# Optimization experiments

Hardware: AMD Instinct MI355X
Metric: run time of the kernel (lower is better)

Reference implementation:

```python
import jax, jax.numpy as jnp
import numpy as np

N, P, T, K = 20000, 5, 16, 3
IN, H, O = 150, 64, 128


def setup_inputs() -> dict:
    key = jax.random.key(0)
    k1, k2, k3, k4, k5 = jax.random.split(key, 5)
    x = jax.random.normal(k1, (N, IN), dtype=jnp.float32)
    conn_idx = jax.random.randint(k2, (N, P, T, K), 0, N, dtype=jnp.int32)
    conn_w = jax.random.uniform(k3, (N, P, T, K), dtype=jnp.float32)
    # learned params
    W1 = jax.random.normal(k4, (H, IN), dtype=jnp.float32) * 0.05   # linear_1 (no bias)
    Wg = jax.random.normal(k5, (O, H, P, T), dtype=jnp.float32) * 0.05  # geodesic conv weight
    bg = jnp.zeros((O,), dtype=jnp.float32)                          # geodesic conv bias
    return {"x": x, "conn_idx": conn_idx, "conn_w": conn_w, "W1": W1, "Wg": Wg, "bg": bg}


def reference(x, conn_idx, conn_w, W1, Wg, bg):
    # Linear + ReLU: [N, H]
    h = jax.nn.relu(x @ W1.T)
    # Geodesic patch gather: interpolate vertex features into P x T bins
    g = jnp.take(h, conn_idx, axis=0)                 # [N, P, T, K, H]
    patches = jnp.einsum('nptk,nptkh->npth', conn_w, g)  # [N, P, T, H]
    # Geodesic convolution: contract patch bins and channels
    out = jnp.einsum('npth,ohpt->no', patches, Wg) + bg  # [N, O]
    # L2 normalize per vertex
    norm = jnp.linalg.norm(out, axis=-1, keepdims=True)
    return out / norm
```

## Files before the change

kernel.cpp:

```cpp
#include <hip/hip_runtime.h>
#include <hip/hip_fp16.h>

#define NV   20000
#define KK   3
#define INF  150
#define HH   64
#define OO   128
#define PT   80
#define KTOT 5120
#define NB   128
#define RS   72
#define CB   (NB * RS)
#define XS   168
#define NBIN 20

typedef _Float16 fh8 __attribute__((ext_vector_type(8)));
typedef __attribute__((ext_vector_type(4))) float f32x4;
typedef __attribute__((ext_vector_type(8))) unsigned short u16x8;

__device__ __forceinline__ unsigned short f2h(float f) {
    return __half_as_ushort(__float2half(f));
}
__device__ __forceinline__ float h2f(unsigned short u) {
    return __half2float(__ushort_as_half(u));
}
__device__ __forceinline__ _Float16 u2h(unsigned short u) {
    union { unsigned short s; _Float16 h; } c; c.s = u; return c.h;
}

__global__ __launch_bounds__(256) void prep_kernel(
    const float* __restrict__ Wg, const float* __restrict__ x,
    const float* __restrict__ W1, unsigned short* __restrict__ W2,
    unsigned short* __restrict__ hb) {
    __shared__ __align__(16) unsigned char smem[32256];
    const int tid = threadIdx.x;

    if (blockIdx.x < 128) {
        float* lds = (float*)smem;
        const int o = blockIdx.x;
        const float* src = Wg + o * KTOT;
        for (int t = tid; t < KTOT; t += 256) {
            int h = t / 80, bin = t - h * 80;
            lds[h * 81 + bin] = src[t];
        }
        __syncthreads();
        for (int t = tid; t < KTOT; t += 256) {
            W2[(t >> 5) * 4096 + o * 32 + (t & 31)] =
                f2h(lds[(t & 63) * 81 + (t >> 6)]);
        }
        return;
    }

    unsigned short* xs = (unsigned short*)smem;
    unsigned short* ws = xs + 32 * XS;
    const int n0 = (blockIdx.x - 128) * 32;

    for (int e = tid; e < 32 * INF; e += 256) {
        int r = e / INF, c = e - r * INF;
        xs[r * XS + c] = f2h(x[n0 * INF + e]);
    }
    for (int e = tid; e < 32 * 18; e += 256) {
        int r = e / 18, c = e - r * 18;
        xs[r * XS + 150 + c] = 0;
    }
    for (int e = tid; e < 64 * INF; e += 256) {
        int r = e / INF, c = e - r * INF;
        ws[r * XS + c] = f2h(W1[e]);
    }
    for (int e = tid; e < 64 * 18; e += 256) {
        int r = e / 18, c = e - r * 18;
        ws[r * XS + 150 + c] = 0;
    }
    __syncthreads();

    const int wv   = tid >> 6;
    const int lane = tid & 63;
    const int q    = lane >> 4;
    const int r16  = lane & 15;
    const int o0   = wv * 16;

    f32x4 acc0 = {0.f, 0.f, 0.f, 0.f};
    f32x4 acc1 = acc0;
    #pragma unroll
    for (int s = 0; s < 5; s++) {
        const int kb = s * 32 + q * 8;
        fh8 a0 = *(const fh8*)(xs + r16 * XS + kb);
        fh8 a1 = *(const fh8*)(xs + (16 + r16) * XS + kb);
        fh8 b  = *(const fh8*)(ws + (o0 + r16) * XS + kb);
        acc0 = __builtin_amdgcn_mfma_f32_16x16x32_f16(a0, b, acc0, 0, 0, 0);
        acc1 = __builtin_amdgcn_mfma_f32_16x16x32_f16(a1, b, acc1, 0, 0, 0);
    }
    #pragma unroll
    for (int r = 0; r < 4; r++) {
        float v0 = acc0[r] > 0.f ? acc0[r] : 0.f;
        float v1 = acc1[r] > 0.f ? acc1[r] : 0.f;
        hb[(n0 + q * 4 + r) * HH + o0 + r16]      = f2h(v0);
        hb[(n0 + 16 + q * 4 + r) * HH + o0 + r16] = f2h(v1);
    }
}

__global__ __launch_bounds__(512, 4) void geo_kernel(
    const int*   __restrict__ conn_idx, const float* __restrict__ conn_w,
    const unsigned short* __restrict__ W2, const unsigned short* __restrict__ hb,
    float* __restrict__ out, unsigned short* __restrict__ parts) {
    __shared__ __align__(16) unsigned short pch[2 * CB];
    __shared__ __align__(16) unsigned short cp[NB * NBIN * 8];

    const int tid  = threadIdx.x;
    const int ks   = blockIdx.x & 3;
    const int n0   = (blockIdx.x >> 2) * NB;
    const int wv   = tid >> 6;
    const int lane = tid & 63;
    const int q    = lane >> 4;
    const int r16  = lane & 15;
    const int j8   = tid & 7;
    const int v0   = tid >> 3;
    const int bbase = ks * NBIN;
    const int Sbase = ks * 40;

    for (int e = tid; e < NB * NBIN; e += 512) {
        const int v = e / NBIN, cc = e - v * NBIN;
        const int vv = n0 + v;
        u16x8 pk = {0, 0, 0, 0, 0, 0, 0, 0};
        if (vv < NV) {
            const int g = vv * (PT * KK) + (bbase + cc) * KK;
            pk[0] = (unsigned short)conn_idx[g];
            pk[1] = (unsigned short)conn_idx[g + 1];
            pk[2] = (unsigned short)conn_idx[g + 2];
            pk[3] = f2h(conn_w[g]);
            pk[4] = f2h(conn_w[g + 1]);
            pk[5] = f2h(conn_w[g + 2]);
        }
        *(u16x8*)(cp + e * 8) = pk;
    }

    f32x4 acc[8];
    #pragma unroll
    for (int m = 0; m < 8; m++) acc[m] = (f32x4){0.f, 0.f, 0.f, 0.f};

    u16x8 pa, pb;
    fh8   hva0, hva1, hva2, hvb0, hvb1, hvb2;

    auto loadg = [&](int cc) {
        pa = *(const u16x8*)(cp + (v0 * NBIN + cc) * 8);
        pb = *(const u16x8*)(cp + ((v0 + 64) * NBIN + cc) * 8);
        hva0 = *(const fh8*)(hb + (int)pa[0] * HH + j8 * 8);
        hva1 = *(const fh8*)(hb + (int)pa[1] * HH + j8 * 8);
        hva2 = *(const fh8*)(hb + (int)pa[2] * HH + j8 * 8);
        hvb0 = *(const fh8*)(hb + (int)pb[0] * HH + j8 * 8);
        hvb1 = *(const fh8*)(hb + (int)pb[1] * HH + j8 * 8);
        hvb2 = *(const fh8*)(hb + (int)pb[2] * HH + j8 * 8);
    };
    auto w2ld = [&](int cc, fh8& b0, fh8& b1) {
        const unsigned short* wp =
            W2 + (Sbase + cc * 2) * 4096 + (wv * 16 + r16) * 32 + q * 8;
        b0 = *(const fh8*)(wp);
        b1 = *(const fh8*)(wp + 4096);
    };
    auto cwr = [&](unsigned short* buf) {
        const _Float16 a0 = u2h(pa[3]), a1 = u2h(pa[4]), a2 = u2h(pa[5]);
        const _Float16 b0 = u2h(pb[3]), b1 = u2h(pb[4]), b2 = u2h(pb[5]);
        const fh8 A0 = {a0, a0, a0, a0, a0, a0, a0, a0};
        const fh8 A1 = {a1, a1, a1, a1, a1, a1, a1, a1};
        const fh8 A2 = {a2, a2, a2, a2, a2, a2, a2, a2};
        const fh8 B0 = {b0, b0, b0, b0, b0, b0, b0, b0};
        const fh8 B1 = {b1, b1, b1, b1, b1, b1, b1, b1};
        const fh8 B2 = {b2, b2, b2, b2, b2, b2, b2, b2};
        fh8 ra = hva0 * A0 + hva1 * A1 + hva2 * A2;
        fh8 rb = hvb0 * B0 + hvb1 * B1 + hvb2 * B2;
        *(fh8*)(buf + v0 * RS + j8 * 8)        = ra;
        *(fh8*)(buf + (v0 + 64) * RS + j8 * 8) = rb;
    };
    auto mfmaph = [&](const unsigned short* buf, fh8 w0, fh8 w1) {
        #pragma unroll
        for (int s = 0; s < 2; s++) {
            const int ao = s * 32 + q * 8;
            const fh8 bf = s ? w1 : w0;
            #pragma unroll
            for (int m = 0; m < 8; m++) {
                fh8 af = *(const fh8*)(buf + (m * 16 + r16) * RS + ao);
                acc[m] = __builtin_amdgcn_mfma_f32_16x16x32_f16(af, bf, acc[m], 0, 0, 0);
            }
        }
    };

    __syncthreads();

    fh8 w2a0, w2a1, w2b0, w2b1;
    loadg(0);
    w2ld(0, w2a0, w2a1);
    cwr(pch);
    __syncthreads();

    #pragma unroll 1
    for (int cc = 0; cc < NBIN; cc += 2) {
        loadg(cc + 1);
        w2ld(cc + 1, w2b0, w2b1);
        mfmaph(pch, w2a0, w2a1);
        cwr(pch + CB);
        __syncthreads();
        if (cc + 2 < NBIN) {
            loadg(cc + 2);
            w2ld(cc + 2, w2a0, w2a1);
        }
        mfmaph(pch + CB, w2b0, w2b1);
        if (cc + 2 < NBIN) cwr(pch);
        __syncthreads();
    }

    if (ks == 0) {
        #pragma unroll
        for (int m = 0; m < 8; m++) {
            const int rb = n0 + m * 16 + q * 4;
            #pragma unroll
            for (int r = 0; r < 4; r++) {
                if (rb + r < NV)
                    out[(rb + r) * OO + wv * 16 + r16] = acc[m][r];
            }
        }
    } else {
        unsigned short* pp = parts + (ks - 1) * (NV * OO);
        #pragma unroll
        for (int m = 0; m < 8; m++) {
            const int rb = n0 + m * 16 + q * 4;
            #pragma unroll
            for (int r = 0; r < 4; r++) {
                if (rb + r < NV)
                    pp[(rb + r) * OO + wv * 16 + r16] = f2h(acc[m][r]);
            }
        }
    }
}

__global__ __launch_bounds__(256) void norm_kernel(
    float* __restrict__ out, const unsigned short* __restrict__ parts,
    const float* __restrict__ bg) {
    const int tid = threadIdx.x;
    const int n   = blockIdx.x * 32 + (tid >> 3);
    const int l   = tid & 7;
    float v[16];
    float s = 0.f;
    #pragma unroll
    for (int i = 0; i < 16; i++) {
        const int o = i * 8 + l;
        const int e = n * OO + o;
        v[i] = out[e] + h2f(parts[e]) + h2f(parts[NV * OO + e]) +
               h2f(parts[2 * NV * OO + e]) + bg[o];
        s += v[i] * v[i];
    }
    for (int off = 4; off; off >>= 1) s += __shfl_down(s, off, 8);
    const float r = rsqrtf(__shfl(s, 0, 8));
    #pragma unroll
    for (int i = 0; i < 16; i++)
        out[n * OO + i * 8 + l] = v[i] * r;
}

extern "C" void kernel_launch(void* const* d_in, const int* in_sizes, int n_in,
                              void* d_out, int out_size, void* d_ws, size_t ws_size,
                              hipStream_t stream) {
    const float* x        = (const float*)d_in[0];
    const int*   conn_idx = (const int*)  d_in[1];
    const float* conn_w   = (const float*)d_in[2];
    const float* W1       = (const float*)d_in[3];
    const float* Wg       = (const float*)d_in[4];
    const float* bg       = (const float*)d_in[5];
    float*       out      = (float*)d_out;

    unsigned short* W2    = (unsigned short*)d_ws;
    unsigned short* hb    = W2 + OO * KTOT;
    unsigned short* parts = hb + NV * HH;

    const int vtiles = (NV + NB - 1) / NB;

    hipLaunchKernelGGL(prep_kernel, dim3(128 + NV / 32), dim3(256), 0, stream,
                       Wg, x, W1, W2, hb);
    hipLaunchKernelGGL(geo_kernel, dim3(4 * vtiles), dim3(512), 0, stream,
                       conn_idx, conn_w, W2, hb, out, parts);
    hipLaunchKernelGGL(norm_kernel, dim3(NV / 32), dim3(256), 0, stream,
                       out, parts, bg);
}
```

Before: 172.8 us.

## Enlarge geo tile to 160 vertices, halve connectivity smem, reload W2 per phase

```diff
diff --git a/kernel.cpp b/kernel.cpp
--- a/kernel.cpp
+++ b/kernel.cpp
@@ -8,11 +8,12 @@
 #define OO   128
 #define PT   80
 #define KTOT 5120
-#define NB   128
+#define NB   160
 #define RS   72
 #define CB   (NB * RS)
 #define XS   168
 #define NBIN 20
+#define NCH  10
 
 typedef _Float16 fh8 __attribute__((ext_vector_type(8)));
 typedef __attribute__((ext_vector_type(4))) float f32x4;
@@ -104,7 +105,7 @@
     const unsigned short* __restrict__ W2, const unsigned short* __restrict__ hb,
     float* __restrict__ out, unsigned short* __restrict__ parts) {
     __shared__ __align__(16) unsigned short pch[2 * CB];
-    __shared__ __align__(16) unsigned short cp[NB * NBIN * 8];
+    __shared__ __align__(16) unsigned short cp[NB * NCH * 8];
 
     const int tid  = threadIdx.x;
     const int ks   = blockIdx.x & 3;
@@ -115,47 +116,68 @@
     const int r16  = lane & 15;
     const int j8   = tid & 7;
     const int v0   = tid >> 3;
+    const bool lo  = (tid < 256);
     const int bbase = ks * NBIN;
     const int Sbase = ks * 40;
 
-    for (int e = tid; e < NB * NBIN; e += 512) {
-        const int v = e / NBIN, cc = e - v * NBIN;
-        const int vv = n0 + v;
-        u16x8 pk = {0, 0, 0, 0, 0, 0, 0, 0};
-        if (vv < NV) {
-            const int g = vv * (PT * KK) + (bbase + cc) * KK;
+    for (int e = tid; e < NB * NCH; e += 512) {
+        const int v = e / NCH, cc = e - v * NCH;
+        const int g = (n0 + v) * (PT * KK) + (bbase + cc) * KK;
+        u16x8 pk;
+        pk[0] = (unsigned short)conn_idx[g];
+        pk[1] = (unsigned short)conn_idx[g + 1];
+        pk[2] = (unsigned short)conn_idx[g + 2];
+        pk[3] = f2h(conn_w[g]);
+        pk[4] = f2h(conn_w[g + 1]);
+        pk[5] = f2h(conn_w[g + 2]);
+        pk[6] = 0; pk[7] = 0;
+        *(u16x8*)(cp + e * 8) = pk;
+    }
+
+    u16x8 cpre0, cpre1, cpre2, cpre3 = {0, 0, 0, 0, 0, 0, 0, 0};
+    {
+        auto packc = [&](int e) {
+            const int v = e / NCH, cc = e - v * NCH;
+            const int g = (n0 + v) * (PT * KK) + (bbase + NCH + cc) * KK;
+            u16x8 pk;
             pk[0] = (unsigned short)conn_idx[g];
             pk[1] = (unsigned short)conn_idx[g + 1];
             pk[2] = (unsigned short)conn_idx[g + 2];
             pk[3] = f2h(conn_w[g]);
             pk[4] = f2h(conn_w[g + 1]);
             pk[5] = f2h(conn_w[g + 2]);
-        }
-        *(u16x8*)(cp + e * 8) = pk;
-    }
-
-    f32x4 acc[8];
-    #pragma unroll
-    for (int m = 0; m < 8; m++) acc[m] = (f32x4){0.f, 0.f, 0.f, 0.f};
-
-    u16x8 pa, pb;
-    fh8   hva0, hva1, hva2, hvb0, hvb1, hvb2;
+            pk[6] = 0; pk[7] = 0;
+            return pk;
+        };
+        cpre0 = packc(tid);
+        cpre1 = packc(tid + 512);
+        cpre2 = packc(tid + 1024);
+        if (tid < NB * NCH - 1536) cpre3 = packc(tid + 1536);
+    }
+
+    f32x4 acc[10];
+    #pragma unroll
+    for (int m = 0; m < 10; m++) acc[m] = (f32x4){0.f, 0.f, 0.f, 0.f};
+
+    u16x8 pa, pb, pc;
+    fh8   hva0, hva1, hva2, hvb0, hvb1, hvb2, hvc0, hvc1, hvc2;
 
     auto loadg = [&](int cc) {
-        pa = *(const u16x8*)(cp + (v0 * NBIN + cc) * 8);
-        pb = *(const u16x8*)(cp + ((v0 + 64) * NBIN + cc) * 8);
+        const int bb = (cc >= NCH) ? cc - NCH : cc;
+        pa = *(const u16x8*)(cp + (v0 * NCH + bb) * 8);
+        pb = *(const u16x8*)(cp + ((v0 + 64) * NCH + bb) * 8);
         hva0 = *(const fh8*)(hb + (int)pa[0] * HH + j8 * 8);
         hva1 = *(const fh8*)(hb + (int)pa[1] * HH + j8 * 8);
         hva2 = *(const fh8*)(hb + (int)pa[2] * HH + j8 * 8);
         hvb0 = *(const fh8*)(hb + (int)pb[0] * HH + j8 * 8);
         hvb1 = *(const fh8*)(hb + (int)pb[1] * HH + j8 * 8);
         hvb2 = *(const fh8*)(hb + (int)pb[2] * HH + j8 * 8);
-    };
-    auto w2ld = [&](int cc, fh8& b0, fh8& b1) {
-        const unsigned short* wp =
-            W2 + (Sbase + cc * 2) * 4096 + (wv * 16 + r16) * 32 + q * 8;
-        b0 = *(const fh8*)(wp);
-        b1 = *(const fh8*)(wp + 4096);
+        if (lo) {
+            pc = *(const u16x8*)(cp + ((v0 + 128) * NCH + bb) * 8);
+            hvc0 = *(const fh8*)(hb + (int)pc[0] * HH + j8 * 8);
+            hvc1 = *(const fh8*)(hb + (int)pc[1] * HH + j8 * 8);
+            hvc2 = *(const fh8*)(hb + (int)pc[2] * HH + j8 * 8);
+        }
     };
     auto cwr = [&](unsigned short* buf) {
         const _Float16 a0 = u2h(pa[3]), a1 = u2h(pa[4]), a2 = u2h(pa[5]);
@@ -170,14 +192,26 @@
         fh8 rb = hvb0 * B0 + hvb1 * B1 + hvb2 * B2;
         *(fh8*)(buf + v0 * RS + j8 * 8)        = ra;
         *(fh8*)(buf + (v0 + 64) * RS + j8 * 8) = rb;
+        if (lo) {
+            const _Float16 c0 = u2h(pc[3]), c1 = u2h(pc[4]), c2 = u2h(pc[5]);
+            const fh8 C0 = {c0, c0, c0, c0, c0, c0, c0, c0};
+            const fh8 C1 = {c1, c1, c1, c1, c1, c1, c1, c1};
+            const fh8 C2 = {c2, c2, c2, c2, c2, c2, c2, c2};
+            fh8 rc = hvc0 * C0 + hvc1 * C1 + hvc2 * C2;
+            *(fh8*)(buf + (v0 + 128) * RS + j8 * 8) = rc;
+        }
     };
-    auto mfmaph = [&](const unsigned short* buf, fh8 w0, fh8 w1) {
+    auto mfmaph = [&](const unsigned short* buf, int cc) {
+        const unsigned short* wp =
+            W2 + (Sbase + cc * 2) * 4096 + (wv * 16 + r16) * 32 + q * 8;
+        const fh8 bf0 = *(const fh8*)(wp);
+        const fh8 bf1 = *(const fh8*)(wp + 4096);
         #pragma unroll
         for (int s = 0; s < 2; s++) {
             const int ao = s * 32 + q * 8;
-            const fh8 bf = s ? w1 : w0;
+            const fh8 bf = s ? bf1 : bf0;
             #pragma unroll
-            for (int m = 0; m < 8; m++) {
+            for (int m = 0; m < 10; m++) {
                 fh8 af = *(const fh8*)(buf + (m * 16 + r16) * RS + ao);
                 acc[m] = __builtin_amdgcn_mfma_f32_16x16x32_f16(af, bf, acc[m], 0, 0, 0);
             }
@@ -186,48 +220,42 @@
 
     __syncthreads();
 
-    fh8 w2a0, w2a1, w2b0, w2b1;
     loadg(0);
-    w2ld(0, w2a0, w2a1);
     cwr(pch);
     __syncthreads();
 
     #pragma unroll 1
-    for (int cc = 0; cc < NBIN; cc += 2) {
-        loadg(cc + 1);
-        w2ld(cc + 1, w2b0, w2b1);
-        mfmaph(pch, w2a0, w2a1);
-        cwr(pch + CB);
-        __syncthreads();
-        if (cc + 2 < NBIN) {
-            loadg(cc + 2);
-            w2ld(cc + 2, w2a0, w2a1);
-        }
-        mfmaph(pch + CB, w2b0, w2b1);
-        if (cc + 2 < NBIN) cwr(pch);
+    for (int cc = 0; cc < NBIN; cc++) {
+        if (cc == NCH - 1) {
+            *(u16x8*)(cp + tid * 8)          = cpre0;
+            *(u16x8*)(cp + (tid + 512) * 8)  = cpre1;
+            *(u16x8*)(cp + (tid + 1024) * 8) = cpre2;
+            if (tid < NB * NCH - 1536)
+                *(u16x8*)(cp + (tid + 1536) * 8) = cpre3;
+            __syncthreads();
+        }
+        if (cc + 1 < NBIN) loadg(cc + 1);
+        mfmaph(&pch[(cc & 1) * CB], cc);
+        if (cc + 1 < NBIN) cwr(&pch[((cc + 1) & 1) * CB]);
         __syncthreads();
     }
 
     if (ks == 0) {
         #pragma unroll
-        for (int m = 0; m < 8; m++) {
+        for (int m = 0; m < 10; m++) {
             const int rb = n0 + m * 16 + q * 4;
             #pragma unroll
-            for (int r = 0; r < 4; r++) {
-                if (rb + r < NV)
-                    out[(rb + r) * OO + wv * 16 + r16] = acc[m][r];
-            }
+            for (int r = 0; r < 4; r++)
+                out[(rb + r) * OO + wv * 16 + r16] = acc[m][r];
         }
     } else {
         unsigned short* pp = parts + (ks - 1) * (NV * OO);
         #pragma unroll
-        for (int m = 0; m < 8; m++) {
+        for (int m = 0; m < 10; m++) {
             const int rb = n0 + m * 16 + q * 4;
             #pragma unroll
-            for (int r = 0; r < 4; r++) {
-                if (rb + r < NV)
-                    pp[(rb + r) * OO + wv * 16 + r16] = f2h(acc[m][r]);
-            }
+            for (int r = 0; r < 4; r++)
+                pp[(rb + r) * OO + wv * 16 + r16] = f2h(acc[m][r]);
         }
     }
 }
@@ -270,11 +298,9 @@
     unsigned short* hb    = W2 + OO * KTOT;
     unsigned short* parts = hb + NV * HH;
 
-    const int vtiles = (NV + NB - 1) / NB;
-
     hipLaunchKernelGGL(prep_kernel, dim3(128 + NV / 32), dim3(256), 0, stream,
                        Wg, x, W1, W2, hb);
-    hipLaunchKernelGGL(geo_kernel, dim3(4 * vtiles), dim3(512), 0, stream,
+    hipLaunchKernelGGL(geo_kernel, dim3(4 * (NV / NB)), dim3(512), 0, stream,
                        conn_idx, conn_w, W2, hb, out, parts);
     hipLaunchKernelGGL(norm_kernel, dim3(NV / 32), dim3(256), 0, stream,
                        out, parts, bg);
```

New measurement: 159.0 us. -8.0%, faster.
